# Optimization experiments

Hardware: AMD Instinct MI355X
Metric: run time of the kernel (lower is better)

Reference implementation:

```python
import jax, jax.numpy as jnp
from jax import lax
import numpy as np

N_FEAT = 64
EMB = 128
HID = 2 * EMB  # 256
B, T = 256, 512


def _uniform(key, shape, bound):
    return jax.random.uniform(key, shape, jnp.float32, -bound, bound)


def setup_inputs() -> dict:
    key = jax.random.key(0)
    ks = jax.random.split(key, 9)
    x = jax.random.normal(ks[0], (B, T, N_FEAT), jnp.float32)
    b1 = 1.0 / np.sqrt(HID)
    b2 = 1.0 / np.sqrt(EMB)
    return {
        "x": x,
        "Wih1": _uniform(ks[1], (4 * HID, N_FEAT), b1),
        "Whh1": _uniform(ks[2], (4 * HID, HID), b1),
        "bih1": _uniform(ks[3], (4 * HID,), b1),
        "bhh1": _uniform(ks[4], (4 * HID,), b1),
        "Wih2": _uniform(ks[5], (4 * EMB, HID), b2),
        "Whh2": _uniform(ks[6], (4 * EMB, EMB), b2),
        "bih2": _uniform(ks[7], (4 * EMB,), b2),
        "bhh2": _uniform(ks[8], (4 * EMB,), b2),
    }


def lstm_layer(x, Wih, Whh, bih, bhh):
    """Single-layer batch_first LSTM, PyTorch gate order (i, f, g, o)."""
    Bb = x.shape[0]
    H = Whh.shape[1]
    # Precompute input contribution for all timesteps: [B, T, 4H]
    xg = jnp.einsum('bti,gi->btg', x, Wih) + bih + bhh

    def step(carry, g_t):
        h, c = carry
        gates = g_t + h @ Whh.T  # [B, 4H]
        i, f, g, o = jnp.split(gates, 4, axis=-1)
        i = jax.nn.sigmoid(i)
        f = jax.nn.sigmoid(f)
        g = jnp.tanh(g)
        o = jax.nn.sigmoid(o)
        c = f * c + i * g
        h = o * jnp.tanh(c)
        return (h, c), h

    h0 = jnp.zeros((Bb, H), x.dtype)
    (_, _), hs = lax.scan(step, (h0, h0), jnp.swapaxes(xg, 0, 1))  # hs: [T, B, H]
    return jnp.swapaxes(hs, 0, 1)


def reference(x, Wih1, Whh1, bih1, bhh1, Wih2, Whh2, bih2, bhh2):
    h1 = lstm_layer(x, Wih1, Whh1, bih1, bhh1)   # [B, T, 2E]
    h2 = lstm_layer(h1, Wih2, Whh2, bih2, bhh2)  # [B, T, E]
    return h2, h2[:, -1, :]
```

## Files before the change

### kernel.cpp

```cpp
#include <hip/hip_runtime.h>

typedef _Float16 half8 __attribute__((ext_vector_type(8)));
typedef float f32x4 __attribute__((ext_vector_type(4)));
typedef unsigned long long ull;

typedef ull      __attribute__((may_alias)) ull_a;
typedef unsigned __attribute__((may_alias)) u32_a;
typedef float4   __attribute__((may_alias)) float4_a;

#define LGKM_BAR() asm volatile("s_waitcnt lgkmcnt(0)" ::: "memory")

#define Bb 256
#define Tt 512
#define NF 64
#define H1u 256
#define H2u 128
#define NGRP 16
#define Bs 16
#define NBLK 64
#define NTHR 256

#define NF1 10
#define NF2 12
#define NT1 4
#define NT2 2

#define OFFB_WF1 0
#define SZB_WF1  (16*4*NF1*64*16)
#define OFFB_WF2 (OFFB_WF1+SZB_WF1)
#define SZB_WF2  (16*2*NF2*64*16)
#define OFFB_BF1 (OFFB_WF2+SZB_WF2)
#define SZB_BF1  (16*4*4*4*4)
#define OFFB_BF2 (OFFB_BF1+SZB_BF1)
#define SZB_BF2  (16*2*4*4*4)
#define OFFB_PH1 (OFFB_BF2+SZB_BF2)
#define SZB_PH1  (2*16*8192)
#define OFFB_PH2 (OFFB_PH1+SZB_PH1)
#define SZB_PH2  (2*16*4096)
#define OFFB_STM (OFFB_PH2+SZB_PH2)
#define SZB_STM  (16*256)

__device__ __forceinline__ float sigf(float x) {
    return 1.0f / (1.0f + __expf(-x));
}
__device__ __forceinline__ float tanhfast(float x) {
    return 2.0f / (1.0f + __expf(-2.0f * x)) - 1.0f;
}

__global__ __launch_bounds__(256) void prep4(
    const float* __restrict__ Wih1, const float* __restrict__ Whh1,
    const float* __restrict__ bih1, const float* __restrict__ bhh1,
    const float* __restrict__ Wih2, const float* __restrict__ Whh2,
    const float* __restrict__ bih2, const float* __restrict__ bhh2,
    char* __restrict__ wsb)
{
    _Float16* wf1 = (_Float16*)(wsb + OFFB_WF1);
    _Float16* wf2 = (_Float16*)(wsb + OFFB_WF2);
    float*    bf1 = (float*)(wsb + OFFB_BF1);
    float*    bf2 = (float*)(wsb + OFFB_BF2);
    const int stride = gridDim.x * blockDim.x;
    const int i0 = blockIdx.x * blockDim.x + threadIdx.x;

    for (int idx = i0; idx < 16*4*NF1*64; idx += stride) {
        const int lane = idx & 63;
        int q = idx >> 6;
        const int f = q % NF1;  q /= NF1;
        const int tt = q & 3;
        const int w  = q >> 2;
        const int r = lane & 15;
        const int unit = w*16 + tt*4 + (r >> 2);
        const int gate = r & 3;
        const int grow = gate * H1u + unit;
        _Float16* dst = wf1 + (size_t)idx * 8;
        #pragma unroll
        for (int e = 0; e < 8; ++e) {
            const int k = f*32 + (lane >> 4)*8 + e;
            const float v = (k < NF) ? Wih1[grow*NF + k]
                                     : Whh1[grow*H1u + (k - NF)];
            dst[e] = (_Float16)v;
        }
    }
    for (int idx = i0; idx < 16*2*NF2*64; idx += stride) {
        const int lane = idx & 63;
        int q = idx >> 6;
        const int f = q % NF2;  q /= NF2;
        const int tt = q & 1;
        const int w  = q >> 1;
        const int r = lane & 15;
        const int unit = w*8 + tt*4 + (r >> 2);
        const int gate = r & 3;
        const int grow = gate * H2u + unit;
        _Float16* dst = wf2 + (size_t)idx * 8;
        #pragma unroll
        for (int e = 0; e < 8; ++e) {
            const int k = f*32 + (lane >> 4)*8 + e;
            const float v = (k < H1u) ? Wih2[grow*H1u + k]
                                      : Whh2[grow*H2u + (k - H1u)];
            dst[e] = (_Float16)v;
        }
    }
    for (int idx = i0; idx < 16*4*4*4; idx += stride) {
        const int reg = idx & 3, lg = (idx >> 2) & 3;
        const int tt = (idx >> 4) & 3, w = idx >> 6;
        const int unit = w*16 + tt*4 + lg;
        const int grow = reg * H1u + unit;
        bf1[idx] = bih1[grow] + bhh1[grow];
    }
    for (int idx = i0; idx < 16*2*4*4; idx += stride) {
        const int reg = idx & 3, lg = (idx >> 2) & 3;
        const int tt = (idx >> 4) & 1, w = idx >> 5;
        const int unit = w*8 + tt*4 + lg;
        const int grow = reg * H2u + unit;
        bf2[idx] = bih2[grow] + bhh2[grow];
    }
}

__device__ __forceinline__ void load_x_frags(half8* xf, const float* __restrict__ x,
                                             int b0, int b, int g, int t)
{
    #pragma unroll
    for (int f = 0; f < 2; ++f) {
        const float* xp = x + (((size_t)(b0 + b)) * Tt + t) * NF + f * 32 + g * 8;
        const float4 lo = *(const float4*)xp;
        const float4 hi = *(const float4*)(xp + 4);
        half8 v;
        v[0] = (_Float16)lo.x; v[1] = (_Float16)lo.y;
        v[2] = (_Float16)lo.z; v[3] = (_Float16)lo.w;
        v[4] = (_Float16)hi.x; v[5] = (_Float16)hi.y;
        v[6] = (_Float16)hi.z; v[7] = (_Float16)hi.w;
        xf[f] = v;
    }
}

__global__ __launch_bounds__(NTHR, 1) void lstm_v7(
    const float* __restrict__ x, char* wsb, float* __restrict__ out)
{
    __shared__ char ldsraw[4 * 2048];

    const int tid   = threadIdx.x;
    const int w     = tid >> 6;
    const int lane  = tid & 63;
    const int g     = lane >> 4;
    const int b     = lane & 15;
    const int grp   = blockIdx.x & 15;
    const int slice = blockIdx.x >> 4;
    const int W     = slice * 4 + w;
    const int b0    = grp * Bs;

    const _Float16* wf1g = (const _Float16*)(wsb + OFFB_WF1);
    const _Float16* wf2g = (const _Float16*)(wsb + OFFB_WF2);
    const float*    bf1g = (const float*)(wsb + OFFB_BF1);
    const float*    bf2g = (const float*)(wsb + OFFB_BF2);
    ull*            ph1  = (ull*)(wsb + OFFB_PH1);
    ull*            ph2  = (ull*)(wsb + OFFB_PH2);
    unsigned*       pu2  = (unsigned*)(wsb + OFFB_PH2);
    unsigned*       stm  = (unsigned*)(wsb + OFFB_STM) + grp * 64;

    char* myl = ldsraw + w * 2048;
    _Float16* l_h1 = (_Float16*)(myl);
    _Float16* l_h2 = (_Float16*)(myl + 512);
    float*    l_o  = (float*)(myl + 1024);

    half8 wA1[NT1][NF1];
    half8 wA2[NT2][NF2];
    #pragma unroll
    for (int tt = 0; tt < NT1; ++tt)
        #pragma unroll
        for (int f = 0; f < NF1; ++f)
            wA1[tt][f] = *(const half8*)(wf1g + ((size_t)(((W*4 + tt)*NF1 + f) * 64 + lane)) * 8);
    #pragma unroll
    for (int tt = 0; tt < NT2; ++tt)
        #pragma unroll
        for (int f = 0; f < NF2; ++f)
            wA2[tt][f] = *(const half8*)(wf2g + ((size_t)(((W*2 + tt)*NF2 + f) * 64 + lane)) * 8);

    f32x4 bias1[NT1], bias2[NT2];
    #pragma unroll
    for (int tt = 0; tt < NT1; ++tt)
        bias1[tt] = *(const f32x4*)(bf1g + ((W*4 + tt)*4 + g) * 4);
    #pragma unroll
    for (int tt = 0; tt < NT2; ++tt)
        bias2[tt] = *(const f32x4*)(bf2g + ((W*2 + tt)*4 + g) * 4);

    float c1s[NT1] = {0.f, 0.f, 0.f, 0.f};
    float c2s[NT2] = {0.f, 0.f};

    half8 hz = {};
    half8 hf[8]  = {hz, hz, hz, hz, hz, hz, hz, hz};
    half8 h2f[4] = {hz, hz, hz, hz};
    half8 xf[2];
    load_x_frags(xf, x, b0, b, g, 0);

    for (int t = 0; t <= Tt; ++t) {
        if (t < Tt) {
            f32x4 acc[NT1] = {};
            #pragma unroll
            for (int tt = 0; tt < NT1; ++tt) {
                acc[tt] = __builtin_amdgcn_mfma_f32_16x16x32_f16(wA1[tt][0], xf[0], acc[tt], 0, 0, 0);
                acc[tt] = __builtin_amdgcn_mfma_f32_16x16x32_f16(wA1[tt][1], xf[1], acc[tt], 0, 0, 0);
            }
            #pragma unroll
            for (int f = 0; f < 8; ++f)
                #pragma unroll
                for (int tt = 0; tt < NT1; ++tt)
                    acc[tt] = __builtin_amdgcn_mfma_f32_16x16x32_f16(wA1[tt][2 + f], hf[f], acc[tt], 0, 0, 0);
            #pragma unroll
            for (int tt = 0; tt < NT1; ++tt) {
                const float iv = sigf(acc[tt][0] + bias1[tt][0]);
                const float fv = sigf(acc[tt][1] + bias1[tt][1]);
                const float gv = tanhfast(acc[tt][2] + bias1[tt][2]);
                const float ov = sigf(acc[tt][3] + bias1[tt][3]);
                const float c = fmaf(fv, c1s[tt], iv * gv);
                c1s[tt] = c;
                const float h = ov * tanhfast(c);
                const int ul = tt * 4 + g;
                l_h1[((ul >> 3) * 16 + b) * 8 + (ul & 7)] = (_Float16)h;
            }
            LGKM_BAR();
            {
                const ull v = *(const ull_a*)(l_h1 + lane * 4);
                const size_t di = ((size_t)((t & 1) * 16 + grp)) * 1024 + W * 64 + lane;
                __hip_atomic_store(ph1 + di, v, __ATOMIC_RELAXED, __HIP_MEMORY_SCOPE_AGENT);
            }
        }
        if (t >= 1) {
            f32x4 acc[NT2] = {};
            #pragma unroll
            for (int f = 0; f < 8; ++f)
                #pragma unroll
                for (int tt = 0; tt < NT2; ++tt)
                    acc[tt] = __builtin_amdgcn_mfma_f32_16x16x32_f16(wA2[tt][f], hf[f], acc[tt], 0, 0, 0);
            #pragma unroll
            for (int f = 0; f < 4; ++f)
                #pragma unroll
                for (int tt = 0; tt < NT2; ++tt)
                    acc[tt] = __builtin_amdgcn_mfma_f32_16x16x32_f16(wA2[tt][8 + f], h2f[f], acc[tt], 0, 0, 0);
            #pragma unroll
            for (int tt = 0; tt < NT2; ++tt) {
                const float iv = sigf(acc[tt][0] + bias2[tt][0]);
                const float fv = sigf(acc[tt][1] + bias2[tt][1]);
                const float gv = tanhfast(acc[tt][2] + bias2[tt][2]);
                const float ov = sigf(acc[tt][3] + bias2[tt][3]);
                const float c = fmaf(fv, c2s[tt], iv * gv);
                c2s[tt] = c;
                const float h = ov * tanhfast(c);
                const int ul = tt * 4 + g;
                if (t < Tt) l_h2[b * 8 + ul] = (_Float16)h;
                l_o[b * 8 + ul] = h;
            }
            LGKM_BAR();
            if (t < Tt) {
                const unsigned v = *(const u32_a*)((const _Float16*)l_h2 + lane * 2);
                const size_t di = ((size_t)(((t + 1) & 1) * 16 + grp)) * 1024 + W * 64 + lane;
                __hip_atomic_store(pu2 + di, v, __ATOMIC_RELAXED, __HIP_MEMORY_SCOPE_AGENT);
            }
        }
        if (t < Tt) {
            asm volatile("s_waitcnt vmcnt(0)" ::: "memory");
            if (lane == 0)
                __hip_atomic_store(&stm[W], (unsigned)(t + 1),
                                   __ATOMIC_RELAXED, __HIP_MEMORY_SCOPE_AGENT);
        }
        if (t >= 1 && lane < 32) {
            const int s_ = t - 1;
            const int bb = lane >> 1, q = lane & 1;
            const float4 ov = *(const float4_a*)(l_o + bb * 8 + q * 4);
            *(float4*)&out[((size_t)(b0 + bb) * Tt + s_) * H2u + W * 8 + q * 4] = ov;
            if (s_ == Tt - 1)
                *(float4*)&out[(size_t)Bb * Tt * H2u + (size_t)(b0 + bb) * H2u + W * 8 + q * 4] = ov;
        }
        if (t + 1 < Tt) load_x_frags(xf, x, b0, b, g, t + 1);
        if (t < Tt) {
            const int si = lane & 31;
            const unsigned need = (si < 16) ? (unsigned)(t + 1) : (unsigned)t;
            const unsigned* sp = stm + si;
            for (;;) {
                const unsigned v = __hip_atomic_load(sp, __ATOMIC_RELAXED, __HIP_MEMORY_SCOPE_AGENT);
                if (__all((int)(v >= need))) break;
                __builtin_amdgcn_s_sleep(1);
            }
            const size_t base1 = ((size_t)((t & 1) * 16 + grp)) * 1024;
            #pragma unroll
            for (int f = 0; f < 8; ++f) {
                const size_t a = base1 + (size_t)(4 * f + g) * 32 + b * 2;
                union { ull q[2]; half8 h; } u;
                u.q[0] = __hip_atomic_load(ph1 + a,     __ATOMIC_RELAXED, __HIP_MEMORY_SCOPE_AGENT);
                u.q[1] = __hip_atomic_load(ph1 + a + 1, __ATOMIC_RELAXED, __HIP_MEMORY_SCOPE_AGENT);
                hf[f] = u.h;
            }
            const size_t base2 = ((size_t)(((t + 1) & 1) * 16 + grp)) * 512;
            #pragma unroll
            for (int f = 0; f < 4; ++f) {
                const size_t a = base2 + (size_t)(4 * f + g) * 32 + b * 2;
                union { ull q[2]; half8 h; } u;
                u.q[0] = __hip_atomic_load(ph2 + a,     __ATOMIC_RELAXED, __HIP_MEMORY_SCOPE_AGENT);
                u.q[1] = __hip_atomic_load(ph2 + a + 1, __ATOMIC_RELAXED, __HIP_MEMORY_SCOPE_AGENT);
                h2f[f] = u.h;
            }
            asm volatile("s_waitcnt vmcnt(0)" ::: "memory");
            if (lane == 0)
                __hip_atomic_store(&stm[16 + W], (unsigned)(t + 1),
                                   __ATOMIC_RELAXED, __HIP_MEMORY_SCOPE_AGENT);
        }
    }
}

extern "C" void kernel_launch(void* const* d_in, const int* in_sizes, int n_in,
                              void* d_out, int out_size, void* d_ws, size_t ws_size,
                              hipStream_t stream) {
    const float* x    = (const float*)d_in[0];
    const float* Wih1 = (const float*)d_in[1];
    const float* Whh1 = (const float*)d_in[2];
    const float* bih1 = (const float*)d_in[3];
    const float* bhh1 = (const float*)d_in[4];
    const float* Wih2 = (const float*)d_in[5];
    const float* Whh2 = (const float*)d_in[6];
    const float* bih2 = (const float*)d_in[7];
    const float* bhh2 = (const float*)d_in[8];
    char*  wsb = (char*)d_ws;
    float* out = (float*)d_out;

    prep4<<<256, 256, 0, stream>>>(Wih1, Whh1, bih1, bhh1,
                                   Wih2, Whh2, bih2, bhh2, wsb);
    hipMemsetAsync((void*)(wsb + OFFB_PH1), 0, SZB_PH1 + SZB_PH2 + SZB_STM, stream);
    lstm_v7<<<NBLK, NTHR, 0, stream>>>(x, wsb, out);
}
```

Before: 2.061 ms.

## Process two batch groups per block and drop the read-done handshake

The kernel now launches 32 blocks instead of 64. Each block handles two 16-row batch groups in an interleaved loop, so the same register-resident weights serve both groups. The inter-block spin wait now checks only the producer step counters, and the separate consumer 'read complete' flag store is gone, which removes one flag round-trip per step. In exchange, each wave does twice the MFMA and activation work on the serial recurrent critical path. The hope is that interleaving the two groups hides latency and that the lighter synchronisation covers the extra work.

Result: slower. 3.924 ms (+90.4%).

```diff
diff --git a/kernel.cpp b/kernel.cpp
--- a/kernel.cpp
+++ b/kernel.cpp
@@ -9,16 +9,15 @@
 typedef float4   __attribute__((may_alias)) float4_a;
 
 #define LGKM_BAR() asm volatile("s_waitcnt lgkmcnt(0)" ::: "memory")
+#define VM_DRAIN() asm volatile("s_waitcnt vmcnt(0)" ::: "memory")
 
 #define Bb 256
 #define Tt 512
 #define NF 64
 #define H1u 256
 #define H2u 128
-#define NGRP 16
-#define Bs 16
-#define NBLK 64
 #define NTHR 256
+#define NBLK 32
 
 #define NF1 10
 #define NF2 12
@@ -132,7 +131,7 @@
     }
 }
 
-__global__ __launch_bounds__(NTHR, 1) void lstm_v7(
+__global__ __launch_bounds__(NTHR, 1) void lstm_v9(
     const float* __restrict__ x, char* wsb, float* __restrict__ out)
 {
     __shared__ char ldsraw[4 * 2048];
@@ -142,10 +141,13 @@
     const int lane  = tid & 63;
     const int g     = lane >> 4;
     const int b     = lane & 15;
-    const int grp   = blockIdx.x & 15;
-    const int slice = blockIdx.x >> 4;
+    const int set   = blockIdx.x & 7;
+    const int slice = blockIdx.x >> 3;
     const int W     = slice * 4 + w;
-    const int b0    = grp * Bs;
+    const int gA    = set * 2;
+    const int gB    = set * 2 + 1;
+    const int b0A   = gA * 16;
+    const int b0B   = gB * 16;
 
     const _Float16* wf1g = (const _Float16*)(wsb + OFFB_WF1);
     const _Float16* wf2g = (const _Float16*)(wsb + OFFB_WF2);
@@ -154,7 +156,8 @@
     ull*            ph1  = (ull*)(wsb + OFFB_PH1);
     ull*            ph2  = (ull*)(wsb + OFFB_PH2);
     unsigned*       pu2  = (unsigned*)(wsb + OFFB_PH2);
-    unsigned*       stm  = (unsigned*)(wsb + OFFB_STM) + grp * 64;
+    unsigned*       stmA = (unsigned*)(wsb + OFFB_STM) + gA * 64;
+    unsigned*       stmB = (unsigned*)(wsb + OFFB_STM) + gB * 64;
 
     char* myl = ldsraw + w * 2048;
     _Float16* l_h1 = (_Float16*)(myl);
@@ -182,125 +185,141 @@
     for (int tt = 0; tt < NT2; ++tt)
         bias2[tt] = *(const f32x4*)(bf2g + ((W*2 + tt)*4 + g) * 4);
 
-    float c1s[NT1] = {0.f, 0.f, 0.f, 0.f};
-    float c2s[NT2] = {0.f, 0.f};
-
     half8 hz = {};
-    half8 hf[8]  = {hz, hz, hz, hz, hz, hz, hz, hz};
-    half8 h2f[4] = {hz, hz, hz, hz};
-    half8 xf[2];
-    load_x_frags(xf, x, b0, b, g, 0);
+    float c1A[NT1] = {0,0,0,0}, c2A[NT2] = {0,0};
+    float c1B[NT1] = {0,0,0,0}, c2B[NT2] = {0,0};
+    half8 hfA[8]  = {hz,hz,hz,hz,hz,hz,hz,hz}, h2fA[4] = {hz,hz,hz,hz};
+    half8 hfB[8]  = {hz,hz,hz,hz,hz,hz,hz,hz}, h2fB[4] = {hz,hz,hz,hz};
+    half8 xfA[2], xfB[2];
+    load_x_frags(xfA, x, b0A, b, g, 0);
+    load_x_frags(xfB, x, b0B, b, g, 0);
 
     for (int t = 0; t <= Tt; ++t) {
+        #pragma unroll
+        for (int gq = 0; gq < 2; ++gq) {
+            const int grp = gq ? gB : gA;
+            const int b0  = gq ? b0B : b0A;
+            half8* hf  = gq ? hfB  : hfA;
+            half8* h2f = gq ? h2fB : h2fA;
+            half8* xf  = gq ? xfB  : xfA;
+            float* c1s = gq ? c1B : c1A;
+            float* c2s = gq ? c2B : c2A;
+            unsigned* stm = gq ? stmB : stmA;
+
+            if (t < Tt) {
+                f32x4 acc[NT1] = {};
+                #pragma unroll
+                for (int tt = 0; tt < NT1; ++tt) {
+                    acc[tt] = __builtin_amdgcn_mfma_f32_16x16x32_f16(wA1[tt][0], xf[0], acc[tt], 0, 0, 0);
+                    acc[tt] = __builtin_amdgcn_mfma_f32_16x16x32_f16(wA1[tt][1], xf[1], acc[tt], 0, 0, 0);
+                }
+                #pragma unroll
+                for (int f = 0; f < 8; ++f)
+                    #pragma unroll
+                    for (int tt = 0; tt < NT1; ++tt)
+                        acc[tt] = __builtin_amdgcn_mfma_f32_16x16x32_f16(wA1[tt][2 + f], hf[f], acc[tt], 0, 0, 0);
+                #pragma unroll
+                for (int tt = 0; tt < NT1; ++tt) {
+                    const float iv = sigf(acc[tt][0] + bias1[tt][0]);
+                    const float fv = sigf(acc[tt][1] + bias1[tt][1]);
+                    const float gv = tanhfast(acc[tt][2] + bias1[tt][2]);
+                    const float ov = sigf(acc[tt][3] + bias1[tt][3]);
+                    const float c = fmaf(fv, c1s[tt], iv * gv);
+                    c1s[tt] = c;
+                    const float h = ov * tanhfast(c);
+                    const int ul = tt * 4 + g;
+                    l_h1[((ul >> 3) * 16 + b) * 8 + (ul & 7)] = (_Float16)h;
+                }
+            }
+            if (t >= 1) {
+                f32x4 acc[NT2] = {};
+                #pragma unroll
+                for (int f = 0; f < 8; ++f)
+                    #pragma unroll
+                    for (int tt = 0; tt < NT2; ++tt)
+                        acc[tt] = __builtin_amdgcn_mfma_f32_16x16x32_f16(wA2[tt][f], hf[f], acc[tt], 0, 0, 0);
+                #pragma unroll
+                for (int f = 0; f < 4; ++f)
+                    #pragma unroll
+                    for (int tt = 0; tt < NT2; ++tt)
+                        acc[tt] = __builtin_amdgcn_mfma_f32_16x16x32_f16(wA2[tt][8 + f], h2f[f], acc[tt], 0, 0, 0);
+                #pragma unroll
+                for (int tt = 0; tt < NT2; ++tt) {
+                    const float iv = sigf(acc[tt][0] + bias2[tt][0]);
+                    const float fv = sigf(acc[tt][1] + bias2[tt][1]);
+                    const float gv = tanhfast(acc[tt][2] + bias2[tt][2]);
+                    const float ov = sigf(acc[tt][3] + bias2[tt][3]);
+                    const float c = fmaf(fv, c2s[tt], iv * gv);
+                    c2s[tt] = c;
+                    const float h = ov * tanhfast(c);
+                    const int ul = tt * 4 + g;
+                    if (t < Tt) l_h2[b * 8 + ul] = (_Float16)h;
+                    l_o[b * 8 + ul] = h;
+                }
+            }
+            LGKM_BAR();
+
+            if (t < Tt) {
+                {
+                    const ull v = *(const ull_a*)(l_h1 + lane * 4);
+                    const size_t di = ((size_t)((t & 1) * 16 + grp)) * 1024 + W * 64 + lane;
+                    __hip_atomic_store(ph1 + di, v, __ATOMIC_RELAXED, __HIP_MEMORY_SCOPE_AGENT);
+                }
+                if (t >= 1) {
+                    const unsigned v = *(const u32_a*)((const _Float16*)l_h2 + lane * 2);
+                    const size_t di = ((size_t)(((t + 1) & 1) * 16 + grp)) * 1024 + W * 64 + lane;
+                    __hip_atomic_store(pu2 + di, v, __ATOMIC_RELAXED, __HIP_MEMORY_SCOPE_AGENT);
+                }
+                VM_DRAIN();
+                if (lane == 0)
+                    __hip_atomic_store(&stm[W], (unsigned)(t + 1),
+                                       __ATOMIC_RELAXED, __HIP_MEMORY_SCOPE_AGENT);
+            }
+            if (t >= 1 && lane < 32) {
+                const int s_ = t - 1;
+                const int bb = lane >> 1, q = lane & 1;
+                const float4 ov = *(const float4_a*)(l_o + bb * 8 + q * 4);
+                *(float4*)&out[((size_t)(b0 + bb) * Tt + s_) * H2u + W * 8 + q * 4] = ov;
+                if (s_ == Tt - 1)
+                    *(float4*)&out[(size_t)Bb * Tt * H2u + (size_t)(b0 + bb) * H2u + W * 8 + q * 4] = ov;
+            }
+            if (t + 1 < Tt) load_x_frags(xf, x, b0, b, g, t + 1);
+        }
+
         if (t < Tt) {
-            f32x4 acc[NT1] = {};
             #pragma unroll
-            for (int tt = 0; tt < NT1; ++tt) {
-                acc[tt] = __builtin_amdgcn_mfma_f32_16x16x32_f16(wA1[tt][0], xf[0], acc[tt], 0, 0, 0);
-                acc[tt] = __builtin_amdgcn_mfma_f32_16x16x32_f16(wA1[tt][1], xf[1], acc[tt], 0, 0, 0);
-            }
-            #pragma unroll
-            for (int f = 0; f < 8; ++f)
-                #pragma unroll
-                for (int tt = 0; tt < NT1; ++tt)
-                    acc[tt] = __builtin_amdgcn_mfma_f32_16x16x32_f16(wA1[tt][2 + f], hf[f], acc[tt], 0, 0, 0);
-            #pragma unroll
-            for (int tt = 0; tt < NT1; ++tt) {
-                const float iv = sigf(acc[tt][0] + bias1[tt][0]);
-                const float fv = sigf(acc[tt][1] + bias1[tt][1]);
-                const float gv = tanhfast(acc[tt][2] + bias1[tt][2]);
-                const float ov = sigf(acc[tt][3] + bias1[tt][3]);
-                const float c = fmaf(fv, c1s[tt], iv * gv);
-                c1s[tt] = c;
-                const float h = ov * tanhfast(c);
-                const int ul = tt * 4 + g;
-                l_h1[((ul >> 3) * 16 + b) * 8 + (ul & 7)] = (_Float16)h;
-            }
-            LGKM_BAR();
-            {
-                const ull v = *(const ull_a*)(l_h1 + lane * 4);
-                const size_t di = ((size_t)((t & 1) * 16 + grp)) * 1024 + W * 64 + lane;
-                __hip_atomic_store(ph1 + di, v, __ATOMIC_RELAXED, __HIP_MEMORY_SCOPE_AGENT);
-            }
-        }
-        if (t >= 1) {
-            f32x4 acc[NT2] = {};
-            #pragma unroll
-            for (int f = 0; f < 8; ++f)
-                #pragma unroll
-                for (int tt = 0; tt < NT2; ++tt)
-                    acc[tt] = __builtin_amdgcn_mfma_f32_16x16x32_f16(wA2[tt][f], hf[f], acc[tt], 0, 0, 0);
-            #pragma unroll
-            for (int f = 0; f < 4; ++f)
-                #pragma unroll
-                for (int tt = 0; tt < NT2; ++tt)
-                    acc[tt] = __builtin_amdgcn_mfma_f32_16x16x32_f16(wA2[tt][8 + f], h2f[f], acc[tt], 0, 0, 0);
-            #pragma unroll
-            for (int tt = 0; tt < NT2; ++tt) {
-                const float iv = sigf(acc[tt][0] + bias2[tt][0]);
-                const float fv = sigf(acc[tt][1] + bias2[tt][1]);
-                const float gv = tanhfast(acc[tt][2] + bias2[tt][2]);
-                const float ov = sigf(acc[tt][3] + bias2[tt][3]);
-                const float c = fmaf(fv, c2s[tt], iv * gv);
-                c2s[tt] = c;
-                const float h = ov * tanhfast(c);
-                const int ul = tt * 4 + g;
-                if (t < Tt) l_h2[b * 8 + ul] = (_Float16)h;
-                l_o[b * 8 + ul] = h;
-            }
-            LGKM_BAR();
-            if (t < Tt) {
-                const unsigned v = *(const u32_a*)((const _Float16*)l_h2 + lane * 2);
-                const size_t di = ((size_t)(((t + 1) & 1) * 16 + grp)) * 1024 + W * 64 + lane;
-                __hip_atomic_store(pu2 + di, v, __ATOMIC_RELAXED, __HIP_MEMORY_SCOPE_AGENT);
-            }
-        }
-        if (t < Tt) {
-            asm volatile("s_waitcnt vmcnt(0)" ::: "memory");
-            if (lane == 0)
-                __hip_atomic_store(&stm[W], (unsigned)(t + 1),
-                                   __ATOMIC_RELAXED, __HIP_MEMORY_SCOPE_AGENT);
-        }
-        if (t >= 1 && lane < 32) {
-            const int s_ = t - 1;
-            const int bb = lane >> 1, q = lane & 1;
-            const float4 ov = *(const float4_a*)(l_o + bb * 8 + q * 4);
-            *(float4*)&out[((size_t)(b0 + bb) * Tt + s_) * H2u + W * 8 + q * 4] = ov;
-            if (s_ == Tt - 1)
-                *(float4*)&out[(size_t)Bb * Tt * H2u + (size_t)(b0 + bb) * H2u + W * 8 + q * 4] = ov;
-        }
-        if (t + 1 < Tt) load_x_frags(xf, x, b0, b, g, t + 1);
-        if (t < Tt) {
-            const int si = lane & 31;
-            const unsigned need = (si < 16) ? (unsigned)(t + 1) : (unsigned)t;
-            const unsigned* sp = stm + si;
-            for (;;) {
-                const unsigned v = __hip_atomic_load(sp, __ATOMIC_RELAXED, __HIP_MEMORY_SCOPE_AGENT);
-                if (__all((int)(v >= need))) break;
-                __builtin_amdgcn_s_sleep(1);
-            }
-            const size_t base1 = ((size_t)((t & 1) * 16 + grp)) * 1024;
-            #pragma unroll
-            for (int f = 0; f < 8; ++f) {
-                const size_t a = base1 + (size_t)(4 * f + g) * 32 + b * 2;
-                union { ull q[2]; half8 h; } u;
-                u.q[0] = __hip_atomic_load(ph1 + a,     __ATOMIC_RELAXED, __HIP_MEMORY_SCOPE_AGENT);
-                u.q[1] = __hip_atomic_load(ph1 + a + 1, __ATOMIC_RELAXED, __HIP_MEMORY_SCOPE_AGENT);
-                hf[f] = u.h;
-            }
-            const size_t base2 = ((size_t)(((t + 1) & 1) * 16 + grp)) * 512;
-            #pragma unroll
-            for (int f = 0; f < 4; ++f) {
-                const size_t a = base2 + (size_t)(4 * f + g) * 32 + b * 2;
-                union { ull q[2]; half8 h; } u;
-                u.q[0] = __hip_atomic_load(ph2 + a,     __ATOMIC_RELAXED, __HIP_MEMORY_SCOPE_AGENT);
-                u.q[1] = __hip_atomic_load(ph2 + a + 1, __ATOMIC_RELAXED, __HIP_MEMORY_SCOPE_AGENT);
-                h2f[f] = u.h;
-            }
-            asm volatile("s_waitcnt vmcnt(0)" ::: "memory");
-            if (lane == 0)
-                __hip_atomic_store(&stm[16 + W], (unsigned)(t + 1),
-                                   __ATOMIC_RELAXED, __HIP_MEMORY_SCOPE_AGENT);
+            for (int gq = 0; gq < 2; ++gq) {
+                const int grp = gq ? gB : gA;
+                half8* hf  = gq ? hfB  : hfA;
+                half8* h2f = gq ? h2fB : h2fA;
+                unsigned* stm = gq ? stmB : stmA;
+
+                const unsigned* sp = stm + ((lane < 16) ? lane : 0);
+                const unsigned need = (lane < 16) ? (unsigned)(t + 1) : 0u;
+                for (;;) {
+                    const unsigned v = __hip_atomic_load(sp, __ATOMIC_RELAXED, __HIP_MEMORY_SCOPE_AGENT);
+                    if (__all((int)(v >= need))) break;
+                    __builtin_amdgcn_s_sleep(1);
+                }
+                const size_t base1 = ((size_t)((t & 1) * 16 + grp)) * 1024;
+                #pragma unroll
+                for (int f = 0; f < 8; ++f) {
+                    const size_t a = base1 + (size_t)(4 * f + g) * 32 + b * 2;
+                    union { ull q[2]; half8 h; } u;
+                    u.q[0] = __hip_atomic_load(ph1 + a,     __ATOMIC_RELAXED, __HIP_MEMORY_SCOPE_AGENT);
+                    u.q[1] = __hip_atomic_load(ph1 + a + 1, __ATOMIC_RELAXED, __HIP_MEMORY_SCOPE_AGENT);
+                    hf[f] = u.h;
+                }
+                const size_t base2 = ((size_t)(((t + 1) & 1) * 16 + grp)) * 512;
+                #pragma unroll
+                for (int f = 0; f < 4; ++f) {
+                    const size_t a = base2 + (size_t)(4 * f + g) * 32 + b * 2;
+                    union { ull q[2]; half8 h; } u;
+                    u.q[0] = __hip_atomic_load(ph2 + a,     __ATOMIC_RELAXED, __HIP_MEMORY_SCOPE_AGENT);
+                    u.q[1] = __hip_atomic_load(ph2 + a + 1, __ATOMIC_RELAXED, __HIP_MEMORY_SCOPE_AGENT);
+                    h2f[f] = u.h;
+                }
+            }
         }
     }
 }
@@ -323,5 +342,5 @@
     prep4<<<256, 256, 0, stream>>>(Wih1, Whh1, bih1, bhh1,
                                    Wih2, Whh2, bih2, bhh2, wsb);
     hipMemsetAsync((void*)(wsb + OFFB_PH1), 0, SZB_PH1 + SZB_PH2 + SZB_STM, stream);
-    lstm_v7<<<NBLK, NTHR, 0, stream>>>(x, wsb, out);
-}
+    lstm_v9<<<NBLK, NTHR, 0, stream>>>(x, wsb, out);
+}
```
